# Performance work log

Hardware: AMD Instinct MI355X
Metric: run time of the kernel (lower is better)

## Reference

```python
import jax, jax.numpy as jnp
import numpy as np

H, DH = 16, 64            # heads, dim_head (rope dim == DH)
NUM_CHAINS = 2
TWO_PI = 2.0 * np.pi
LN_EPS = 1e-5


def layer_norm(x, gamma):
    mu = jnp.mean(x, axis=-1, keepdims=True)
    var = jnp.var(x, axis=-1, keepdims=True)
    return (x - mu) * jax.lax.rsqrt(var + LN_EPS) * gamma


def rotate_half(x):
    # pairs are interleaved: (..., d*2) viewed as (..., d, 2); (x1,x2)->(-x2,x1)
    x1 = x[..., 0::2]
    x2 = x[..., 1::2]
    return jnp.stack((-x2, x1), axis=-1).reshape(x.shape)


def cyclic_rope_freqs(residue_index, chain_index, cyclic_mask, rope_freqs, dtype):
    """Angles [B,L,DH]: standard RoPE (with chain-offset combination) for linear
    tokens, ring harmonics omega_i = 2*pi*k_i/L_chain for cyclic tokens."""
    t = residue_index.astype(dtype)                      # B L (interpolate_factor=1)
    ci = chain_index.astype(dtype)
    F = rope_freqs.shape[0]                              # DH//2 = 32
    # standard path (RotaryEmbedding._forward with chain_index):
    # residue_indices = arange(F)%F = identity; chain_indices = arange(F)//F = 0
    res = t[..., None] * rope_freqs                      # B L F
    ch0 = ci * rope_freqs[0]                             # B L  (chain_freqs[...,0])
    std = jnp.repeat(res + ch0[..., None], 2, axis=-1)   # B L DH (interleaved repeat)
    # ring size per token: count of cyclic tokens on each token's chain
    oh = jax.nn.one_hot(chain_index, NUM_CHAINS, dtype=dtype)        # B L C
    counts = jnp.einsum('blc,bl->bc', oh, cyclic_mask)               # B C
    ring = jnp.take_along_axis(counts, chain_index, axis=1) * cyclic_mask  # B L
    ring_safe = jnp.maximum(ring, 1.0)
    max_k = jnp.maximum(jnp.floor(ring_safe * 0.5), 1.0)             # B L
    kk = jnp.arange(1, F + 1, dtype=dtype)
    k_eff = jnp.where(max_k[..., None] == 1.0, 1.0,
                      1.0 + jnp.mod(kk - 1.0, max_k[..., None]))     # B L F
    omega = TWO_PI * k_eff / ring_safe[..., None]                    # B L F
    cyc = jnp.repeat(omega * t[..., None], 2, axis=-1)               # B L DH
    return jnp.where((cyclic_mask > 0)[..., None], cyc, std)


def setup_inputs() -> dict:
    key = jax.random.key(0)
    ks = jax.random.split(key, 8)
    B, L, dim = 4, 1024, 1024
    s = 0.02
    x = jax.random.normal(ks[0], (B, L, dim), jnp.float32)
    time = jax.random.normal(ks[1], (B, 1, dim), jnp.float32)
    seq_mask = jnp.ones((B, L), jnp.float32)
    residue_index = (jnp.arange(B * L, dtype=jnp.int32).reshape(B, L)) % L
    chain_index = jax.random.randint(ks[2], (B, L), 0, NUM_CHAINS).astype(jnp.int32)
    cyclic_mask = jax.random.randint(ks[3], (B, L), 0, 2).astype(jnp.float32)
    gamma = jnp.ones((dim,), jnp.float32)
    Wt = jax.random.normal(ks[4], (2 * dim, dim), jnp.float32) * s
    bt = jnp.zeros((2 * dim,), jnp.float32)
    Wq = jax.random.normal(ks[5], (H * DH, dim), jnp.float32) * s
    Wkv = jax.random.normal(ks[6], (2 * H * DH, dim), jnp.float32) * s
    Wo = jax.random.normal(ks[7], (dim, H * DH), jnp.float32) * s
    rope_freqs = 1.0 / (10000.0 ** (jnp.arange(0, DH, 2, dtype=jnp.float32) / DH))
    return {"x": x, "time": time, "seq_mask": seq_mask, "cyclic_mask": cyclic_mask,
            "gamma": gamma, "Wt": Wt, "bt": bt, "Wq": Wq, "Wkv": Wkv, "Wo": Wo,
            "rope_freqs": rope_freqs,
            "residue_index": residue_index, "chain_index": chain_index}


def reference(x, time, seq_mask, cyclic_mask, gamma, Wt, bt, Wq, Wkv, Wo,
              rope_freqs, residue_index, chain_index):
    B, L, dim = x.shape
    x = x * seq_mask[..., None]
    xn = layer_norm(x, gamma)
    # time conditioning: SiLU -> Linear -> (scale, shift)
    ss = jax.nn.silu(time) @ Wt.T + bt                   # B 1 2*dim
    scale, shift = jnp.split(ss, 2, axis=-1)
    xc = xn * (scale + 1.0) + shift                      # B L dim
    q = (xc @ Wq.T).reshape(B, L, H, DH).transpose(0, 2, 1, 3)   # B H L Dh
    k, v = jnp.split(xc @ Wkv.T, 2, axis=-1)
    k = k.reshape(B, L, H, DH).transpose(0, 2, 1, 3)
    v = v.reshape(B, L, H, DH).transpose(0, 2, 1, 3)
    # cyclic rotary embeddings (full head dim rotated)
    freqs = cyclic_rope_freqs(residue_index, chain_index, cyclic_mask,
                              rope_freqs, x.dtype)        # B L DH
    cos_f = jnp.cos(freqs)[:, None]                       # B 1 L DH
    sin_f = jnp.sin(freqs)[:, None]
    q = q * cos_f + rotate_half(q) * sin_f
    k = k * cos_f + rotate_half(k) * sin_f
    sim = jnp.einsum('bhid,bhjd->bhij', q * (DH ** -0.5), k)
    neg = -jnp.finfo(sim.dtype).max
    sim = jnp.where(seq_mask[:, None, None, :] > 0, sim, neg)
    attn = jax.nn.softmax(sim, axis=-1)
    out = jnp.einsum('bhij,bhjd->bhid', attn, v)
    out = out.transpose(0, 2, 1, 3).reshape(B, L, H * DH)
    out = out @ Wo.T
    return out * seq_mask[..., None]
```

## Files before the change

### kernel.cpp

```cpp
#include <hip/hip_runtime.h>
#include <hip/hip_bf16.h>
#include <math.h>

#define NB 4
#define NL 1024
#define NDIM 1024
#define NH 16
#define NDH 64
#define NEG_MAX (-3.402823466e38f)

typedef __attribute__((ext_vector_type(4))) float fx4;
typedef __attribute__((ext_vector_type(8))) short bh8;

__device__ __forceinline__ ushort f2bf(float f){
    __hip_bfloat16 h = __float2bfloat16(f);
    return *(ushort*)&h;
}
__device__ __forceinline__ float bf2f(ushort h){
    return __uint_as_float(((unsigned)h)<<16);
}
__device__ __forceinline__ void gload16(const void* g, void* l){
    __builtin_amdgcn_global_load_lds((const __attribute__((address_space(1))) void*)g,
                                     (__attribute__((address_space(3))) void*)l, 16, 0, 0);
}

__global__ __launch_bounds__(256) void k_pre1(const float* __restrict__ time_, const float* __restrict__ Wt,
                                              const float* __restrict__ bt, float* __restrict__ ss,
                                              const int* __restrict__ chain, const float* __restrict__ cyc,
                                              float* __restrict__ counts,
                                              const float* __restrict__ Wq, const float* __restrict__ Wkv,
                                              const float* __restrict__ Wo,
                                              ushort* __restrict__ wqkv, ushort* __restrict__ wo){
    __shared__ float red[4];
    int bx = blockIdx.x, t = threadIdx.x;
    if (bx < 2048){
        int gw   = (bx*256 + t) >> 6;
        int lane = t & 63;
        int b = gw >> 11, j = gw & 2047;
        const float* a = time_ + b*NDIM;
        const float* w = Wt + (size_t)j*NDIM;
        float s = 0.f;
        #pragma unroll 4
        for (int i = lane; i < NDIM; i += 64){
            float v = a[i];
            s += (v / (1.f + __expf(-v))) * w[i];
        }
        #pragma unroll
        for (int off=32; off; off>>=1) s += __shfl_xor(s, off, 64);
        if (!lane) ss[gw] = s + bt[j];
    } else if (bx < 2056){
        int cb = bx - 2048;
        int b = cb >> 1, c = cb & 1;
        float s = 0.f;
        for (int l = t; l < NL; l += 256)
            s += (chain[b*NL+l]==c) ? cyc[b*NL+l] : 0.f;
        #pragma unroll
        for (int off=32; off; off>>=1) s += __shfl_xor(s, off, 64);
        if (!(t & 63)) red[t>>6] = s;
        __syncthreads();
        if (!t) counts[cb] = red[0]+red[1]+red[2]+red[3];
    } else {
        int i = ((bx-2056)*256 + t)*4;
        const float* src; ushort* dst;
        if (i < 3145728){
            dst = wqkv + i;
            src = (i < 1048576) ? (Wq + i) : (Wkv + (i - 1048576));
        } else {
            dst = wo + (i - 3145728);
            src = Wo + (i - 3145728);
        }
        fx4 v = *(const fx4*)src;
        ushort4 o; o.x=f2bf(v.x); o.y=f2bf(v.y); o.z=f2bf(v.z); o.w=f2bf(v.w);
        *(ushort4*)dst = o;
    }
}

__global__ __launch_bounds__(256) void k_pre2(const int* __restrict__ resi, const int* __restrict__ chain,
                                              const float* __restrict__ cyc, const float* __restrict__ rf,
                                              const float* __restrict__ counts,
                                              float* __restrict__ cosb, float* __restrict__ sinb,
                                              const float* __restrict__ x, const float* __restrict__ sm,
                                              const float* __restrict__ gamma, const float* __restrict__ ss,
                                              ushort* __restrict__ xc){
    __shared__ float r1[4], r2[4];
    int bx = blockIdx.x, t = threadIdx.x;
    if (bx < 512){
        int idx = bx*256 + t;
        int f  = idx & 31;
        int bl = idx >> 5;
        int b  = bl >> 10;
        float tt = (float)resi[bl];
        int   ci = chain[bl];
        float cm = cyc[bl];
        float ang;
        if (cm > 0.f) {
            float ring      = counts[b*2+ci] * cm;
            float ring_safe = fmaxf(ring, 1.f);
            float max_k     = fmaxf(floorf(ring_safe*0.5f), 1.f);
            float k_eff     = (max_k == 1.f) ? 1.f : (1.f + fmodf((float)f, max_k));
            float omega     = 6.28318530717958647692f * k_eff / ring_safe;
            ang = omega * tt;
        } else {
            ang = tt * rf[f] + (float)ci * rf[0];
        }
        cosb[idx] = cosf(ang);
        sinb[idx] = sinf(ang);
    } else {
        int row = bx - 512;
        int b   = row >> 10;
        float msk = sm[row];
        fx4 v = ((const fx4*)(x + (size_t)row*NDIM))[t];
        v.x*=msk; v.y*=msk; v.z*=msk; v.w*=msk;
        float s1 = v.x+v.y+v.z+v.w;
        float s2 = v.x*v.x + v.y*v.y + v.z*v.z + v.w*v.w;
        #pragma unroll
        for (int off=32; off; off>>=1){ s1 += __shfl_xor(s1,off,64); s2 += __shfl_xor(s2,off,64); }
        if (!(t & 63)){ r1[t>>6]=s1; r2[t>>6]=s2; }
        __syncthreads();
        s1 = r1[0]+r1[1]+r1[2]+r1[3];
        s2 = r2[0]+r2[1]+r2[2]+r2[3];
        float mu  = s1 * (1.f/NDIM);
        float var = s2 * (1.f/NDIM) - mu*mu;
        float rs  = rsqrtf(var + 1e-5f);
        const float* sc = ss + b*2048;
        fx4 g   = ((const fx4*)gamma)[t];
        fx4 scl = ((const fx4*)sc)[t];
        fx4 sh  = ((const fx4*)(sc+1024))[t];
        ushort4 ob;
        ob.x = f2bf((v.x-mu)*rs*g.x*(1.f+scl.x)+sh.x);
        ob.y = f2bf((v.y-mu)*rs*g.y*(1.f+scl.y)+sh.y);
        ob.z = f2bf((v.z-mu)*rs*g.z*(1.f+scl.z)+sh.z);
        ob.w = f2bf((v.w-mu)*rs*g.w*(1.f+scl.w)+sh.w);
        *(ushort4*)(xc + (size_t)row*NDIM + t*4) = ob;
    }
}

template<int MODE>
__global__ __launch_bounds__(256) void k_mm(const ushort* __restrict__ A, const ushort* __restrict__ W,
                                            ushort* __restrict__ qo, ushort* __restrict__ ko,
                                            ushort* __restrict__ vo,
                                            float* __restrict__ outf, const float* __restrict__ smask){
    __shared__ ushort As[2][128*32];
    __shared__ ushort Bs[2][128*32];
    int t = threadIdx.x, l = t&63, w = t>>6;
    int lo = l&15, hi = l>>4;
    const int nbx = (MODE==0) ? 24 : 8;
    const int nwg = (MODE==0) ? 768 : 256;
    int lin = blockIdx.y*nbx + blockIdx.x;
    int swz = (lin & 7)*(nwg>>3) + (lin>>3);
    int m0 = (swz/nbx)*128, n0 = (swz%nbx)*128;
    int wm = (w>>1)*64, wn = (w&1)*64;
    fx4 acc[4][4];
    #pragma unroll
    for (int i=0;i<4;i++)
        #pragma unroll
        for (int j=0;j<4;j++) acc[i][j] = (fx4){0.f,0.f,0.f,0.f};
    const char* Ab = (const char*)A;
    const char* Wb = (const char*)W;

    #define MMSTAGE(bb, k0) { \
        _Pragma("unroll") \
        for (int e=0;e<2;e++){ \
            int c = t + e*256; \
            int row = c>>2, cw = c&3; \
            gload16(Ab + (size_t)(m0+row)*2048 + (k0)*2 + cw*16, (char*)As[bb] + c*16); \
            gload16(Wb + (size_t)(n0+row)*2048 + (k0)*2 + cw*16, (char*)Bs[bb] + c*16); \
        } }

    MMSTAGE(0, 0);
    __syncthreads();
    for (int kt=0; kt<32; kt++){
        int cur = kt & 1;
        if (kt < 31) MMSTAGE(cur^1, (kt+1)*32);
        bh8 af[4], bf[4];
        #pragma unroll
        for (int i=0;i<4;i++) af[i] = *(const bh8*)(&As[cur][0] + (wm + i*16 + lo)*32 + hi*8);
        #pragma unroll
        for (int j=0;j<4;j++) bf[j] = *(const bh8*)(&Bs[cur][0] + (wn + j*16 + lo)*32 + hi*8);
        #pragma unroll
        for (int i=0;i<4;i++)
            #pragma unroll
            for (int j=0;j<4;j++)
                acc[i][j] = __builtin_amdgcn_mfma_f32_16x16x32_bf16(af[i], bf[j], acc[i][j], 0, 0, 0);
        __syncthreads();
    }
    #undef MMSTAGE

    #pragma unroll
    for (int i=0;i<4;i++){
        #pragma unroll
        for (int r=0;r<4;r++){
            int m = m0 + wm + i*16 + hi*4 + r;
            int b_ = m>>10, l_ = m&1023;
            #pragma unroll
            for (int j=0;j<4;j++){
                int n = n0 + wn + j*16 + lo;
                float val = acc[i][j][r];
                if (MODE==0){
                    int nn = n & 1023;
                    int h_ = nn>>6, d_ = nn&63;
                    size_t off = (size_t)((b_*NH + h_)*NL + l_)*NDH + d_;
                    if (n < 1024)      qo[off] = f2bf(val);
                    else if (n < 2048) ko[off] = f2bf(val);
                    else               vo[off] = f2bf(val);
                } else {
                    outf[(size_t)m*NDIM + n] = val * smask[m];
                }
            }
        }
    }
}

__global__ __launch_bounds__(256) void k_mid(ushort* __restrict__ q, ushort* __restrict__ k,
                                             const float* __restrict__ cosb, const float* __restrict__ sinb,
                                             const ushort* __restrict__ v, ushort* __restrict__ vt){
    __shared__ ushort tile[64][65];
    int bx = blockIdx.x, t = threadIdx.x;
    if (bx < 8192){
        int idx = bx*256 + t;
        int f   = idx & 31;
        int bhl = idx >> 5;
        int l   = bhl & 1023;
        int b   = bhl >> 14;
        int ca  = ((b<<10)|l)*32 + f;
        float c = cosb[ca], s = sinb[ca];
        const float QS = 0.18033688011112042f;
        unsigned qp = ((const unsigned*)q)[idx];
        unsigned kp = ((const unsigned*)k)[idx];
        float qx = bf2f((ushort)(qp&0xffffu)), qy = bf2f((ushort)(qp>>16));
        float kx = bf2f((ushort)(kp&0xffffu)), ky = bf2f((ushort)(kp>>16));
        float q0 = (qx*c - qy*s)*QS, q1 = (qy*c + qx*s)*QS;
        float k0 = kx*c - ky*s,      k1 = ky*c + kx*s;
        ((unsigned*)q)[idx] = (unsigned)f2bf(q0) | ((unsigned)f2bf(q1)<<16);
        ((unsigned*)k)[idx] = (unsigned)f2bf(k0) | ((unsigned)f2bf(k1)<<16);
    } else {
        int vb = bx - 8192;
        int bh = vb >> 4, l0 = (vb & 15)*64;
        #pragma unroll
        for (int e=0;e<2;e++){
            int c = t + e*256;
            int row = c>>3, cw = c&7;
            bh8 d = *(const bh8*)(v + ((size_t)bh*NL + l0 + row)*NDH + cw*8);
            #pragma unroll
            for (int x2=0;x2<8;x2++) tile[row][cw*8+x2] = (ushort)d[x2];
        }
        __syncthreads();
        #pragma unroll
        for (int e=0;e<2;e++){
            int c = t + e*256;
            int drow = c>>3, cw = c&7;
            bh8 o;
            #pragma unroll
            for (int x2=0;x2<8;x2++) o[x2] = (short)tile[cw*8+x2][drow];
            *(bh8*)(vt + ((size_t)bh*NDH + drow)*NL + l0 + cw*8) = o;
        }
    }
}

__global__ __launch_bounds__(256) void k_fattn(const ushort* __restrict__ qb, const ushort* __restrict__ kb,
                                               const ushort* __restrict__ vt, const float* __restrict__ smask,
                                               ushort* __restrict__ ao){
    __shared__ ushort Ks[2][64*64];
    __shared__ ushort Vs[2][64*64];
    __shared__ ushort Ps[4][32*64];
    int t = threadIdx.x, l = t&63, w = t>>6;
    int lo = l&15, hi = l>>4;
    int logical = (blockIdx.x & 7)*64 + (blockIdx.x >> 3);
    int bh = logical >> 3;
    int qt = logical & 7;
    int b = bh>>4, h = bh&15;
    int q0 = qt*128;
    int swzq = (lo&7)<<4;

    bh8 aq[2][2];
    #pragma unroll
    for (int qs=0; qs<2; qs++){
        const ushort* qrow = qb + ((size_t)bh*NL + q0 + w*32 + qs*16 + lo)*NDH;
        aq[qs][0] = *(const bh8*)(qrow + hi*8);
        aq[qs][1] = *(const bh8*)(qrow + 32 + hi*8);
    }
    const float* mrow = smask + b*NL;

    fx4 o[2][4];
    float mrun[2], lrun[2];
    #pragma unroll
    for (int qs=0; qs<2; qs++){
        mrun[qs]=NEG_MAX; lrun[qs]=0.f;
        #pragma unroll
        for (int dt=0; dt<4; dt++) o[qs][dt] = (fx4){0.f,0.f,0.f,0.f};
    }

    const char* kbase = (const char*)(kb + (size_t)bh*NL*NDH);
    const char* vbase = (const char*)(vt + (size_t)bh*NDH*NL);

    #define STAGE(bb, jt) { \
        int j0s = (jt)*64; \
        _Pragma("unroll") \
        for (int e=0;e<2;e++){ \
            int c = t + e*256; \
            int row = c>>3, cw = c&7; \
            int lc = cw ^ (row&7); \
            gload16(kbase + (size_t)(j0s+row)*128 + lc*16, (char*)Ks[bb] + c*16); \
        } \
        _Pragma("unroll") \
        for (int e=0;e<2;e++){ \
            int c = t + e*256; \
            int row = c>>3, cw = c&7; \
            int lc = cw ^ (row&7); \
            gload16(vbase + (size_t)row*2048 + j0s*2 + lc*16, (char*)Vs[bb] + c*16); \
        } }

    STAGE(0, 0);
    __syncthreads();

    for (int tt=0; tt<16; ++tt){
        int cur = tt & 1;
        if (tt < 15) STAGE(cur^1, tt+1);
        int j0 = tt*64;
        const char* KsB = (const char*)Ks[cur];
        const char* VsB = (const char*)Vs[cur];
        char* PsB = (char*)&Ps[w][0];

        bh8 kf[4][2];
        #pragma unroll
        for (int j=0;j<4;j++){
            int row = j*16 + lo;
            int swz = (row&7)<<4;
            kf[j][0] = *(const bh8*)(KsB + row*128 + ((hi*16) ^ swz));
            kf[j][1] = *(const bh8*)(KsB + row*128 + ((64 + hi*16) ^ swz));
        }
        fx4 s[2][4];
        __builtin_amdgcn_s_setprio(1);
        #pragma unroll
        for (int qs=0; qs<2; qs++)
            #pragma unroll
            for (int j=0;j<4;j++){
                fx4 z = (fx4){0.f,0.f,0.f,0.f};
                z = __builtin_amdgcn_mfma_f32_16x16x32_bf16(kf[j][0], aq[qs][0], z, 0,0,0);
                z = __builtin_amdgcn_mfma_f32_16x16x32_bf16(kf[j][1], aq[qs][1], z, 0,0,0);
                s[qs][j] = z;
            }
        __builtin_amdgcn_s_setprio(0);
        #pragma unroll
        for (int j=0;j<4;j++){
            float4 mv = *(const float4*)(mrow + j0 + j*16 + hi*4);
            s[0][j][0] = mv.x>0.f ? s[0][j][0] : NEG_MAX;  s[1][j][0] = mv.x>0.f ? s[1][j][0] : NEG_MAX;
            s[0][j][1] = mv.y>0.f ? s[0][j][1] : NEG_MAX;  s[1][j][1] = mv.y>0.f ? s[1][j][1] : NEG_MAX;
            s[0][j][2] = mv.z>0.f ? s[0][j][2] : NEG_MAX;  s[1][j][2] = mv.z>0.f ? s[1][j][2] : NEG_MAX;
            s[0][j][3] = mv.w>0.f ? s[0][j][3] : NEG_MAX;  s[1][j][3] = mv.w>0.f ? s[1][j][3] : NEG_MAX;
        }

        #pragma unroll
        for (int qs=0; qs<2; qs++){
            float m0 = fmaxf(fmaxf(s[qs][0][0], s[qs][0][1]), s[qs][0][2]);
            float m1 = fmaxf(fmaxf(s[qs][0][3], s[qs][1][0]), s[qs][1][1]);
            float m2 = fmaxf(fmaxf(s[qs][1][2], s[qs][1][3]), s[qs][2][0]);
            float m3 = fmaxf(fmaxf(s[qs][2][1], s[qs][2][2]), s[qs][2][3]);
            float m4 = fmaxf(fmaxf(s[qs][3][0], s[qs][3][1]), s[qs][3][2]);
            float mt = fmaxf(fmaxf(fmaxf(m0,m1),m2), fmaxf(fmaxf(m3,m4), s[qs][3][3]));
            mt = fmaxf(mt, __shfl_xor(mt, 16));
            mt = fmaxf(mt, __shfl_xor(mt, 32));
            if (__any(mt > mrun[qs] + 8.f)){
                float mnew = fmaxf(mrun[qs], mt);
                float cc = __builtin_amdgcn_exp2f(mrun[qs] - mnew);
                lrun[qs] *= cc;
                mrun[qs] = mnew;
                #pragma unroll
                for (int r=0;r<4;r++){
                    float ccr = __shfl(cc, hi*4 + r);
                    #pragma unroll
                    for (int dt=0; dt<4; dt++) o[qs][dt][r] *= ccr;
                }
            }
            float p[4][4];
            #pragma unroll
            for (int j=0;j<4;j++)
                #pragma unroll
                for (int r=0;r<4;r++) p[j][r] = __builtin_amdgcn_exp2f(s[qs][j][r] - mrun[qs]);
            float r0 = (p[0][0]+p[0][1]) + (p[0][2]+p[0][3]);
            float r1 = (p[1][0]+p[1][1]) + (p[1][2]+p[1][3]);
            float r2 = (p[2][0]+p[2][1]) + (p[2][2]+p[2][3]);
            float r3 = (p[3][0]+p[3][1]) + (p[3][2]+p[3][3]);
            float rs = (r0+r1)+(r2+r3);
            rs += __shfl_xor(rs, 16);
            rs += __shfl_xor(rs, 32);
            lrun[qs] += rs;
            #pragma unroll
            for (int j=0;j<4;j++){
                uint2 wd;
                wd.x = (unsigned)f2bf(p[j][0]) | ((unsigned)f2bf(p[j][1])<<16);
                wd.y = (unsigned)f2bf(p[j][2]) | ((unsigned)f2bf(p[j][3])<<16);
                *(uint2*)(PsB + (qs*16+lo)*128 + ((j*32 + hi*8) ^ swzq)) = wd;
            }
        }

        bh8 ap[2][2];
        #pragma unroll
        for (int qs=0; qs<2; qs++){
            ap[qs][0] = *(const bh8*)(PsB + (qs*16+lo)*128 + ((hi*16) ^ swzq));
            ap[qs][1] = *(const bh8*)(PsB + (qs*16+lo)*128 + ((64 + hi*16) ^ swzq));
        }
        __builtin_amdgcn_s_setprio(1);
        #pragma unroll
        for (int dt=0; dt<4; dt++){
            int row = dt*16 + lo;
            int swz = (row&7)<<4;
            bh8 bv0 = *(const bh8*)(VsB + row*128 + ((hi*16) ^ swz));
            bh8 bv1 = *(const bh8*)(VsB + row*128 + ((64 + hi*16) ^ swz));
            o[0][dt] = __builtin_amdgcn_mfma_f32_16x16x32_bf16(ap[0][0], bv0, o[0][dt], 0,0,0);
            o[0][dt] = __builtin_amdgcn_mfma_f32_16x16x32_bf16(ap[0][1], bv1, o[0][dt], 0,0,0);
            o[1][dt] = __builtin_amdgcn_mfma_f32_16x16x32_bf16(ap[1][0], bv0, o[1][dt], 0,0,0);
            o[1][dt] = __builtin_amdgcn_mfma_f32_16x16x32_bf16(ap[1][1], bv1, o[1][dt], 0,0,0);
        }
        __builtin_amdgcn_s_setprio(0);
        __syncthreads();
    }
    #undef STAGE

    #pragma unroll
    for (int qs=0; qs<2; qs++){
        float inv = 1.f / lrun[qs];
        #pragma unroll
        for (int r=0;r<4;r++){
            float ivr = __shfl(inv, hi*4 + r);
            int l_ = q0 + w*32 + qs*16 + hi*4 + r;
            size_t base = ((size_t)b*NL + l_)*NDIM + h*NDH;
            #pragma unroll
            for (int dt=0; dt<4; dt++)
                ao[base + dt*16 + lo] = f2bf(o[qs][dt][r] * ivr);
        }
    }
}

extern "C" void kernel_launch(void* const* d_in, const int* in_sizes, int n_in,
                              void* d_out, int out_size, void* d_ws, size_t ws_size,
                              hipStream_t stream) {
    const float* x      = (const float*)d_in[0];
    const float* time_  = (const float*)d_in[1];
    const float* smask  = (const float*)d_in[2];
    const float* cycm   = (const float*)d_in[3];
    const float* gamma  = (const float*)d_in[4];
    const float* Wt     = (const float*)d_in[5];
    const float* bt     = (const float*)d_in[6];
    const float* Wq     = (const float*)d_in[7];
    const float* Wkv    = (const float*)d_in[8];
    const float* Wo     = (const float*)d_in[9];
    const float* rf     = (const float*)d_in[10];
    const int*   resi   = (const int*)d_in[11];
    const int*   chain  = (const int*)d_in[12];
    float* out = (float*)d_out;

    float*  ss     = (float*)d_ws;
    float*  cnts   = ss + 8192;
    float*  cosb   = cnts + 16;
    float*  sinb   = cosb + 131072;
    ushort* xc     = (ushort*)(sinb + 131072);
    ushort* wqkv   = xc + 4194304;
    ushort* wo     = wqkv + 3145728;
    ushort* qbuf   = wo + 1048576;
    ushort* kbuf   = qbuf + 4194304;
    ushort* vbuf   = kbuf + 4194304;
    ushort* vtb    = vbuf + 4194304;
    ushort* aob    = vtb + 4194304;

    hipLaunchKernelGGL(k_pre1,   dim3(6152),   dim3(256), 0, stream,
                       time_, Wt, bt, ss, chain, cycm, cnts, Wq, Wkv, Wo, wqkv, wo);
    hipLaunchKernelGGL(k_pre2,   dim3(4608),   dim3(256), 0, stream,
                       resi, chain, cycm, rf, cnts, cosb, sinb, x, smask, gamma, ss, xc);
    hipLaunchKernelGGL((k_mm<0>), dim3(24,32), dim3(256), 0, stream,
                       xc, wqkv, qbuf, kbuf, vbuf, (float*)nullptr, (const float*)nullptr);
    hipLaunchKernelGGL(k_mid,    dim3(9216),   dim3(256), 0, stream,
                       qbuf, kbuf, cosb, sinb, vbuf, vtb);
    hipLaunchKernelGGL(k_fattn,  dim3(512),    dim3(256), 0, stream,
                       qbuf, kbuf, vtb, smask, aob);
    hipLaunchKernelGGL((k_mm<1>), dim3(8,32),  dim3(256), 0, stream,
                       aob, wo, (ushort*)nullptr, (ushort*)nullptr, (ushort*)nullptr, out, smask);
}
```

Baseline: 220.2 us.

## Fuse RoPE and V transpose into QKV GEMM epilogue, drop k_mid kernel

Removes the separate k_mid kernel. RoPE rotation and the q scale are applied in the QKV GEMM epilogue, using lane shuffles for the interleaved partner and packed cos/sin pairs. V is written already transposed through an LDS staging tile. Both GEMM and attention loops now use explicit vmcnt waits with raw s_barrier instead of __syncthreads, and attention caches the sequence mask in LDS and pads the P buffer. This saves a full read/write pass over q, k and v plus a kernel launch, but makes the epilogue heavier and the pipelining relies on hand-placed waitcnt correctness.

```diff
diff --git a/kernel.cpp b/kernel.cpp
--- a/kernel.cpp
+++ b/kernel.cpp
@@ -78,7 +78,7 @@
 __global__ __launch_bounds__(256) void k_pre2(const int* __restrict__ resi, const int* __restrict__ chain,
                                               const float* __restrict__ cyc, const float* __restrict__ rf,
                                               const float* __restrict__ counts,
-                                              float* __restrict__ cosb, float* __restrict__ sinb,
+                                              float2* __restrict__ cs,
                                               const float* __restrict__ x, const float* __restrict__ sm,
                                               const float* __restrict__ gamma, const float* __restrict__ ss,
                                               ushort* __restrict__ xc){
@@ -103,8 +103,7 @@
         } else {
             ang = tt * rf[f] + (float)ci * rf[0];
         }
-        cosb[idx] = cosf(ang);
-        sinb[idx] = sinf(ang);
+        cs[idx] = make_float2(cosf(ang), sinf(ang));
     } else {
         int row = bx - 512;
         int b   = row >> 10;
@@ -139,9 +138,13 @@
 __global__ __launch_bounds__(256) void k_mm(const ushort* __restrict__ A, const ushort* __restrict__ W,
                                             ushort* __restrict__ qo, ushort* __restrict__ ko,
                                             ushort* __restrict__ vo,
-                                            float* __restrict__ outf, const float* __restrict__ smask){
-    __shared__ ushort As[2][128*32];
-    __shared__ ushort Bs[2][128*32];
+                                            float* __restrict__ outf, const float* __restrict__ smask,
+                                            const float2* __restrict__ cs){
+    union SMem {
+        ushort stage[2][2][128*32];
+        ushort tx[64][136];
+    };
+    __shared__ SMem smem;
     int t = threadIdx.x, l = t&63, w = t>>6;
     int lo = l&15, hi = l>>4;
     const int nbx = (MODE==0) ? 24 : 8;
@@ -163,96 +166,101 @@
         for (int e=0;e<2;e++){ \
             int c = t + e*256; \
             int row = c>>2, cw = c&3; \
-            gload16(Ab + (size_t)(m0+row)*2048 + (k0)*2 + cw*16, (char*)As[bb] + c*16); \
-            gload16(Wb + (size_t)(n0+row)*2048 + (k0)*2 + cw*16, (char*)Bs[bb] + c*16); \
+            gload16(Ab + (size_t)(m0+row)*2048 + (size_t)(k0)*2 + cw*16, (char*)smem.stage[0][bb] + c*16); \
+            gload16(Wb + (size_t)(n0+row)*2048 + (size_t)(k0)*2 + cw*16, (char*)smem.stage[1][bb] + c*16); \
         } }
 
     MMSTAGE(0, 0);
+    asm volatile("s_waitcnt vmcnt(0)" ::: "memory");
     __syncthreads();
     for (int kt=0; kt<32; kt++){
         int cur = kt & 1;
-        if (kt < 31) MMSTAGE(cur^1, (kt+1)*32);
+        MMSTAGE(cur^1, ((kt+1)&31)*32);
+        asm volatile("s_waitcnt vmcnt(4)" ::: "memory");
+        __builtin_amdgcn_s_barrier();
+        __builtin_amdgcn_sched_barrier(0);
         bh8 af[4], bf[4];
         #pragma unroll
-        for (int i=0;i<4;i++) af[i] = *(const bh8*)(&As[cur][0] + (wm + i*16 + lo)*32 + hi*8);
-        #pragma unroll
-        for (int j=0;j<4;j++) bf[j] = *(const bh8*)(&Bs[cur][0] + (wn + j*16 + lo)*32 + hi*8);
+        for (int i=0;i<4;i++) af[i] = *(const bh8*)(&smem.stage[0][cur][0] + (wm + i*16 + lo)*32 + hi*8);
+        #pragma unroll
+        for (int j=0;j<4;j++) bf[j] = *(const bh8*)(&smem.stage[1][cur][0] + (wn + j*16 + lo)*32 + hi*8);
         #pragma unroll
         for (int i=0;i<4;i++)
             #pragma unroll
             for (int j=0;j<4;j++)
                 acc[i][j] = __builtin_amdgcn_mfma_f32_16x16x32_bf16(af[i], bf[j], acc[i][j], 0, 0, 0);
-        __syncthreads();
+        __builtin_amdgcn_s_barrier();
     }
     #undef MMSTAGE
 
-    #pragma unroll
-    for (int i=0;i<4;i++){
-        #pragma unroll
-        for (int r=0;r<4;r++){
-            int m = m0 + wm + i*16 + hi*4 + r;
-            int b_ = m>>10, l_ = m&1023;
-            #pragma unroll
-            for (int j=0;j<4;j++){
-                int n = n0 + wn + j*16 + lo;
-                float val = acc[i][j][r];
-                if (MODE==0){
-                    int nn = n & 1023;
-                    int h_ = nn>>6, d_ = nn&63;
-                    size_t off = (size_t)((b_*NH + h_)*NL + l_)*NDH + d_;
-                    if (n < 1024)      qo[off] = f2bf(val);
-                    else if (n < 2048) ko[off] = f2bf(val);
-                    else               vo[off] = f2bf(val);
-                } else {
-                    outf[(size_t)m*NDIM + n] = val * smask[m];
+    if (MODE==0){
+        if (n0 < 2048){
+            const float qsc = (n0 < 1024) ? 0.18033688011112042f : 1.0f;
+            ushort* dst0 = (n0 < 1024) ? qo : ko;
+            #pragma unroll
+            for (int i=0;i<4;i++){
+                #pragma unroll
+                for (int r=0;r<4;r++){
+                    int m = m0 + wm + i*16 + hi*4 + r;
+                    int b_ = m>>10, l_ = m&1023;
+                    const float2* csrow = cs + (size_t)m*32;
+                    #pragma unroll
+                    for (int j=0;j<4;j++){
+                        int nn = (n0 + wn + j*16 + lo) & 1023;
+                        int h_ = nn>>6, d_ = nn&63;
+                        float2 cspair = csrow[d_>>1];
+                        float val = acc[i][j][r];
+                        float partner = __shfl_xor(val, 1);
+                        float rot = (lo&1) ? fmaf(val, cspair.x,  partner*cspair.y)
+                                           : fmaf(val, cspair.x, -partner*cspair.y);
+                        size_t off = ((size_t)(b_*NH + h_)*NL + l_)*NDH + d_;
+                        dst0[off] = f2bf(rot * qsc);
+                    }
                 }
             }
-        }
-    }
-}
-
-__global__ __launch_bounds__(256) void k_mid(ushort* __restrict__ q, ushort* __restrict__ k,
-                                             const float* __restrict__ cosb, const float* __restrict__ sinb,
-                                             const ushort* __restrict__ v, ushort* __restrict__ vt){
-    __shared__ ushort tile[64][65];
-    int bx = blockIdx.x, t = threadIdx.x;
-    if (bx < 8192){
-        int idx = bx*256 + t;
-        int f   = idx & 31;
-        int bhl = idx >> 5;
-        int l   = bhl & 1023;
-        int b   = bhl >> 14;
-        int ca  = ((b<<10)|l)*32 + f;
-        float c = cosb[ca], s = sinb[ca];
-        const float QS = 0.18033688011112042f;
-        unsigned qp = ((const unsigned*)q)[idx];
-        unsigned kp = ((const unsigned*)k)[idx];
-        float qx = bf2f((ushort)(qp&0xffffu)), qy = bf2f((ushort)(qp>>16));
-        float kx = bf2f((ushort)(kp&0xffffu)), ky = bf2f((ushort)(kp>>16));
-        float q0 = (qx*c - qy*s)*QS, q1 = (qy*c + qx*s)*QS;
-        float k0 = kx*c - ky*s,      k1 = ky*c + kx*s;
-        ((unsigned*)q)[idx] = (unsigned)f2bf(q0) | ((unsigned)f2bf(q1)<<16);
-        ((unsigned*)k)[idx] = (unsigned)f2bf(k0) | ((unsigned)f2bf(k1)<<16);
+        } else {
+            asm volatile("s_waitcnt vmcnt(0)" ::: "memory");
+            __syncthreads();
+            int b_ = m0>>10;
+            #pragma unroll
+            for (int half=0; half<2; half++){
+                if ((w&1) == half){
+                    #pragma unroll
+                    for (int i=0;i<4;i++)
+                        #pragma unroll
+                        for (int r=0;r<4;r++){
+                            int ml = wm + i*16 + hi*4 + r;
+                            #pragma unroll
+                            for (int j=0;j<4;j++){
+                                int nl = (wn + j*16 + lo) & 63;
+                                smem.tx[nl][ml] = f2bf(acc[i][j][r]);
+                            }
+                        }
+                }
+                __syncthreads();
+                int rr = t>>2, qq = t&3;
+                int ng = (n0 - 2048) + half*64 + rr;
+                int h_ = ng>>6, d_ = ng&63;
+                ushort* dst = vo + ((size_t)((b_*NH + h_)*NDH + d_))*NL + (m0 & 1023) + qq*32;
+                #pragma unroll
+                for (int c=0;c<4;c++)
+                    *(bh8*)(dst + c*8) = *(const bh8*)(&smem.tx[rr][qq*32 + c*8]);
+                __syncthreads();
+            }
+        }
     } else {
-        int vb = bx - 8192;
-        int bh = vb >> 4, l0 = (vb & 15)*64;
-        #pragma unroll
-        for (int e=0;e<2;e++){
-            int c = t + e*256;
-            int row = c>>3, cw = c&7;
-            bh8 d = *(const bh8*)(v + ((size_t)bh*NL + l0 + row)*NDH + cw*8);
-            #pragma unroll
-            for (int x2=0;x2<8;x2++) tile[row][cw*8+x2] = (ushort)d[x2];
-        }
-        __syncthreads();
-        #pragma unroll
-        for (int e=0;e<2;e++){
-            int c = t + e*256;
-            int drow = c>>3, cw = c&7;
-            bh8 o;
-            #pragma unroll
-            for (int x2=0;x2<8;x2++) o[x2] = (short)tile[cw*8+x2][drow];
-            *(bh8*)(vt + ((size_t)bh*NDH + drow)*NL + l0 + cw*8) = o;
+        #pragma unroll
+        for (int i=0;i<4;i++){
+            #pragma unroll
+            for (int r=0;r<4;r++){
+                int m = m0 + wm + i*16 + hi*4 + r;
+                float msk = smask[m];
+                #pragma unroll
+                for (int j=0;j<4;j++){
+                    int n = n0 + wn + j*16 + lo;
+                    outf[(size_t)m*NDIM + n] = acc[i][j][r] * msk;
+                }
+            }
         }
     }
 }
@@ -262,7 +270,8 @@
                                                ushort* __restrict__ ao){
     __shared__ ushort Ks[2][64*64];
     __shared__ ushort Vs[2][64*64];
-    __shared__ ushort Ps[4][32*64];
+    __shared__ ushort Ps[4][32*72];
+    __shared__ float  Ms[1024];
     int t = threadIdx.x, l = t&63, w = t>>6;
     int lo = l&15, hi = l>>4;
     int logical = (blockIdx.x & 7)*64 + (blockIdx.x >> 3);
@@ -280,6 +289,7 @@
         aq[qs][1] = *(const bh8*)(qrow + 32 + hi*8);
     }
     const float* mrow = smask + b*NL;
+    gload16((const char*)mrow + t*16, (char*)Ms + t*16);
 
     fx4 o[2][4];
     float mrun[2], lrun[2];
@@ -311,12 +321,17 @@
         } }
 
     STAGE(0, 0);
+    asm volatile("s_waitcnt vmcnt(0)" ::: "memory");
     __syncthreads();
 
     for (int tt=0; tt<16; ++tt){
         int cur = tt & 1;
-        if (tt < 15) STAGE(cur^1, tt+1);
+        STAGE(cur^1, (tt+1)&15);
+        asm volatile("s_waitcnt vmcnt(4)" ::: "memory");
+        __builtin_amdgcn_s_barrier();
+        __builtin_amdgcn_sched_barrier(0);
         int j0 = tt*64;
+
         const char* KsB = (const char*)Ks[cur];
         const char* VsB = (const char*)Vs[cur];
         char* PsB = (char*)&Ps[w][0];
@@ -325,9 +340,9 @@
         #pragma unroll
         for (int j=0;j<4;j++){
             int row = j*16 + lo;
-            int swz = (row&7)<<4;
-            kf[j][0] = *(const bh8*)(KsB + row*128 + ((hi*16) ^ swz));
-            kf[j][1] = *(const bh8*)(KsB + row*128 + ((64 + hi*16) ^ swz));
+            int kswz = (row&7)<<4;
+            kf[j][0] = *(const bh8*)(KsB + row*128 + ((hi*16) ^ kswz));
+            kf[j][1] = *(const bh8*)(KsB + row*128 + ((64 + hi*16) ^ kswz));
         }
         fx4 s[2][4];
         __builtin_amdgcn_s_setprio(1);
@@ -343,7 +358,7 @@
         __builtin_amdgcn_s_setprio(0);
         #pragma unroll
         for (int j=0;j<4;j++){
-            float4 mv = *(const float4*)(mrow + j0 + j*16 + hi*4);
+            float4 mv = *(const float4*)(&Ms[j0 + j*16 + hi*4]);
             s[0][j][0] = mv.x>0.f ? s[0][j][0] : NEG_MAX;  s[1][j][0] = mv.x>0.f ? s[1][j][0] : NEG_MAX;
             s[0][j][1] = mv.y>0.f ? s[0][j][1] : NEG_MAX;  s[1][j][1] = mv.y>0.f ? s[1][j][1] : NEG_MAX;
             s[0][j][2] = mv.z>0.f ? s[0][j][2] : NEG_MAX;  s[1][j][2] = mv.z>0.f ? s[1][j][2] : NEG_MAX;
@@ -352,12 +367,12 @@
 
         #pragma unroll
         for (int qs=0; qs<2; qs++){
-            float m0 = fmaxf(fmaxf(s[qs][0][0], s[qs][0][1]), s[qs][0][2]);
-            float m1 = fmaxf(fmaxf(s[qs][0][3], s[qs][1][0]), s[qs][1][1]);
-            float m2 = fmaxf(fmaxf(s[qs][1][2], s[qs][1][3]), s[qs][2][0]);
-            float m3 = fmaxf(fmaxf(s[qs][2][1], s[qs][2][2]), s[qs][2][3]);
-            float m4 = fmaxf(fmaxf(s[qs][3][0], s[qs][3][1]), s[qs][3][2]);
-            float mt = fmaxf(fmaxf(fmaxf(m0,m1),m2), fmaxf(fmaxf(m3,m4), s[qs][3][3]));
+            float m0_ = fmaxf(fmaxf(s[qs][0][0], s[qs][0][1]), s[qs][0][2]);
+            float m1_ = fmaxf(fmaxf(s[qs][0][3], s[qs][1][0]), s[qs][1][1]);
+            float m2_ = fmaxf(fmaxf(s[qs][1][2], s[qs][1][3]), s[qs][2][0]);
+            float m3_ = fmaxf(fmaxf(s[qs][2][1], s[qs][2][2]), s[qs][2][3]);
+            float m4_ = fmaxf(fmaxf(s[qs][3][0], s[qs][3][1]), s[qs][3][2]);
+            float mt = fmaxf(fmaxf(fmaxf(m0_,m1_),m2_), fmaxf(fmaxf(m3_,m4_), s[qs][3][3]));
             mt = fmaxf(mt, __shfl_xor(mt, 16));
             mt = fmaxf(mt, __shfl_xor(mt, 32));
             if (__any(mt > mrun[qs] + 8.f)){
@@ -390,30 +405,30 @@
                 uint2 wd;
                 wd.x = (unsigned)f2bf(p[j][0]) | ((unsigned)f2bf(p[j][1])<<16);
                 wd.y = (unsigned)f2bf(p[j][2]) | ((unsigned)f2bf(p[j][3])<<16);
-                *(uint2*)(PsB + (qs*16+lo)*128 + ((j*32 + hi*8) ^ swzq)) = wd;
+                *(uint2*)(PsB + (qs*16+lo)*144 + ((j*32 + hi*8) ^ swzq)) = wd;
             }
         }
 
         bh8 ap[2][2];
         #pragma unroll
         for (int qs=0; qs<2; qs++){
-            ap[qs][0] = *(const bh8*)(PsB + (qs*16+lo)*128 + ((hi*16) ^ swzq));
-            ap[qs][1] = *(const bh8*)(PsB + (qs*16+lo)*128 + ((64 + hi*16) ^ swzq));
+            ap[qs][0] = *(const bh8*)(PsB + (qs*16+lo)*144 + ((hi*16) ^ swzq));
+            ap[qs][1] = *(const bh8*)(PsB + (qs*16+lo)*144 + ((64 + hi*16) ^ swzq));
         }
         __builtin_amdgcn_s_setprio(1);
         #pragma unroll
         for (int dt=0; dt<4; dt++){
             int row = dt*16 + lo;
-            int swz = (row&7)<<4;
-            bh8 bv0 = *(const bh8*)(VsB + row*128 + ((hi*16) ^ swz));
-            bh8 bv1 = *(const bh8*)(VsB + row*128 + ((64 + hi*16) ^ swz));
+            int vswz = (row&7)<<4;
+            bh8 bv0 = *(const bh8*)(VsB + row*128 + ((hi*16) ^ vswz));
+            bh8 bv1 = *(const bh8*)(VsB + row*128 + ((64 + hi*16) ^ vswz));
             o[0][dt] = __builtin_amdgcn_mfma_f32_16x16x32_bf16(ap[0][0], bv0, o[0][dt], 0,0,0);
             o[0][dt] = __builtin_amdgcn_mfma_f32_16x16x32_bf16(ap[0][1], bv1, o[0][dt], 0,0,0);
             o[1][dt] = __builtin_amdgcn_mfma_f32_16x16x32_bf16(ap[1][0], bv0, o[1][dt], 0,0,0);
             o[1][dt] = __builtin_amdgcn_mfma_f32_16x16x32_bf16(ap[1][1], bv1, o[1][dt], 0,0,0);
         }
         __builtin_amdgcn_s_setprio(0);
-        __syncthreads();
+        __builtin_amdgcn_s_barrier();
     }
     #undef STAGE
 
@@ -452,27 +467,24 @@
 
     float*  ss     = (float*)d_ws;
     float*  cnts   = ss + 8192;
-    float*  cosb   = cnts + 16;
-    float*  sinb   = cosb + 131072;
-    ushort* xc     = (ushort*)(sinb + 131072);
+    float2* cs     = (float2*)(cnts + 16);
+    ushort* xc     = (ushort*)(cs + 131072);
     ushort* wqkv   = xc + 4194304;
     ushort* wo     = wqkv + 3145728;
     ushort* qbuf   = wo + 1048576;
     ushort* kbuf   = qbuf + 4194304;
-    ushort* vbuf   = kbuf + 4194304;
-    ushort* vtb    = vbuf + 4194304;
+    ushort* vtb    = kbuf + 4194304;
     ushort* aob    = vtb + 4194304;
 
     hipLaunchKernelGGL(k_pre1,   dim3(6152),   dim3(256), 0, stream,
                        time_, Wt, bt, ss, chain, cycm, cnts, Wq, Wkv, Wo, wqkv, wo);
     hipLaunchKernelGGL(k_pre2,   dim3(4608),   dim3(256), 0, stream,
-                       resi, chain, cycm, rf, cnts, cosb, sinb, x, smask, gamma, ss, xc);
+                       resi, chain, cycm, rf, cnts, cs, x, smask, gamma, ss, xc);
     hipLaunchKernelGGL((k_mm<0>), dim3(24,32), dim3(256), 0, stream,
-                       xc, wqkv, qbuf, kbuf, vbuf, (float*)nullptr, (const float*)nullptr);
-    hipLaunchKernelGGL(k_mid,    dim3(9216),   dim3(256), 0, stream,
-                       qbuf, kbuf, cosb, sinb, vbuf, vtb);
+                       xc, wqkv, qbuf, kbuf, vtb, (float*)nullptr, (const float*)nullptr, (const float2*)cs);
     hipLaunchKernelGGL(k_fattn,  dim3(512),    dim3(256), 0, stream,
                        qbuf, kbuf, vtb, smask, aob);
     hipLaunchKernelGGL((k_mm<1>), dim3(8,32),  dim3(256), 0, stream,
-                       aob, wo, (ushort*)nullptr, (ushort*)nullptr, (ushort*)nullptr, out, smask);
-}
+                       aob, wo, (ushort*)nullptr, (ushort*)nullptr, (ushort*)nullptr, out, smask,
+                       (const float2*)nullptr);
+}
```

Result: faster. 212.8 us (-3.4%).
